# Performance work log

Hardware: AMD Instinct MI355X
Metric: run time of the kernel (lower is better)

## Reference

```python
import jax, jax.numpy as jnp
import numpy as np

N = 100000
E = 3200000
F_IN = 27
H1, C1 = 8, 8
H2, C2 = 1, 2
NEG_SLOPE = 0.2


def gat_conv(x, src, dst, W, a_src, a_dst, b, heads, ch, n_nodes):
    # x: [N, F_in]; src/dst: [E'] (self-loops already appended)
    h = (x @ W).reshape(n_nodes, heads, ch)            # [N, H, C]
    alpha_src = jnp.sum(h * a_src, axis=-1)            # [N, H]
    alpha_dst = jnp.sum(h * a_dst, axis=-1)            # [N, H]
    e = jax.nn.leaky_relu(alpha_src[src] + alpha_dst[dst], NEG_SLOPE)  # [E', H]
    m = jax.ops.segment_max(e, dst, num_segments=n_nodes)             # [N, H]
    ex = jnp.exp(e - m[dst])
    denom = jax.ops.segment_sum(ex, dst, num_segments=n_nodes)        # [N, H]
    alpha = ex / denom[dst]                                           # [E', H]
    out = jax.ops.segment_sum(h[src] * alpha[:, :, None], dst, num_segments=n_nodes)
    return out.reshape(n_nodes, heads * ch) + b


def setup_inputs() -> dict:
    key = jax.random.key(0)
    ks = jax.random.split(key, 10)
    x = jax.random.normal(ks[0], (N, F_IN), dtype=jnp.float32)
    edge_index = jax.random.randint(ks[1], (2, E), 0, N, dtype=jnp.int64)
    s1 = 1.0 / np.sqrt(F_IN)
    s2 = 1.0 / np.sqrt(H1 * C1)
    W1 = jax.random.uniform(ks[2], (F_IN, H1 * C1), jnp.float32, -s1, s1)
    a_src1 = jax.random.uniform(ks[3], (H1, C1), jnp.float32, -s1, s1)
    a_dst1 = jax.random.uniform(ks[4], (H1, C1), jnp.float32, -s1, s1)
    b1 = jnp.zeros((H1 * C1,), jnp.float32)
    W2 = jax.random.uniform(ks[5], (H1 * C1, H2 * C2), jnp.float32, -s2, s2)
    a_src2 = jax.random.uniform(ks[6], (H2, C2), jnp.float32, -s2, s2)
    a_dst2 = jax.random.uniform(ks[7], (H2, C2), jnp.float32, -s2, s2)
    b2 = jnp.zeros((H2 * C2,), jnp.float32)
    return {"x": x, "edge_index": edge_index, "W1": W1, "a_src1": a_src1,
            "a_dst1": a_dst1, "b1": b1, "W2": W2, "a_src2": a_src2,
            "a_dst2": a_dst2, "b2": b2}


def reference(x, edge_index, W1, a_src1, a_dst1, b1, W2, a_src2, a_dst2, b2):
    # eval mode: dropouts are identity. PyG GATConv adds self-loops by default.
    loop = jnp.arange(N, dtype=edge_index.dtype)
    src = jnp.concatenate([edge_index[0], loop])
    dst = jnp.concatenate([edge_index[1], loop])
    h = jax.nn.elu(gat_conv(x, src, dst, W1, a_src1, a_dst1, b1, H1, C1, N))
    out = gat_conv(h, src, dst, W2, a_src2, a_dst2, b2, H2, C2, N)
    return jax.nn.log_softmax(out, axis=1)
```

## Files before the change

kernel.cpp:

```cpp
#include <hip/hip_runtime.h>
#include <hip/hip_fp16.h>
#include <math.h>

#define NN 100000
#define EE 3200000
#define ET (EE + NN)

#define H1n 8
#define C1n 8
#define F1n 64
#define FINn 27
#define NEG 0.2f

#define NPB 128
#define NB 782
#define STRIDE 5120
#define TILE 4096
#define ABLK 256
#define WIN (STRIDE + NPB)
#define FBLK 512

typedef float floatx2 __attribute__((ext_vector_type(2)));

static __device__ __forceinline__ float lrelu(float v) {
    return v > 0.f ? v : NEG * v;
}

__global__ __launch_bounds__(ABLK) void k_binA(const int* __restrict__ ei,
                                               int* __restrict__ tail,
                                               int* __restrict__ recs) {
    __shared__ int hist[NB];
    __shared__ int lofs[NB];
    __shared__ int cur[NB];
    __shared__ int gpos[NB];
    __shared__ int sorted[TILE];
    __shared__ unsigned short sbkt[TILE];
    __shared__ int part[ABLK];

    int tid = threadIdx.x;
    long long e0 = (long long)blockIdx.x * TILE;
    int cnt = (int)min((long long)TILE, (long long)EE - e0);

    for (int i = tid; i < NB; i += ABLK) hist[i] = 0;
    __syncthreads();

    int ss[TILE / ABLK], dd[TILE / ABLK];
    #pragma unroll
    for (int k = 0; k < TILE / ABLK; ++k) {
        int idx = k * ABLK + tid;
        if (idx < cnt) {
            ss[k] = ei[e0 + idx];
            dd[k] = ei[EE + e0 + idx];
            atomicAdd(&hist[dd[k] >> 7], 1);
        }
    }
    __syncthreads();
    {
        const int CH = (NB + ABLK - 1) / ABLK;
        int beg = tid * CH, end = min(beg + CH, NB);
        int s = 0;
        for (int i = beg; i < end; ++i) s += hist[i];
        part[tid] = s;
        __syncthreads();
        for (int off = 1; off < ABLK; off <<= 1) {
            int add = (tid >= off) ? part[tid - off] : 0;
            __syncthreads();
            part[tid] += add;
            __syncthreads();
        }
        int ex = (tid > 0) ? part[tid - 1] : 0;
        for (int i = beg; i < end; ++i) {
            lofs[i] = ex;
            cur[i] = ex;
            ex += hist[i];
        }
    }
    __syncthreads();
    #pragma unroll
    for (int k = 0; k < TILE / ABLK; ++k) {
        int idx = k * ABLK + tid;
        if (idx < cnt) {
            int b = dd[k] >> 7;
            int r = atomicAdd(&cur[b], 1);
            sorted[r] = ss[k] | ((dd[k] & (NPB - 1)) << 17);
            sbkt[r] = (unsigned short)b;
        }
    }
    __syncthreads();
    for (int i = tid; i < NB; i += ABLK) {
        int c = hist[i];
        if (c > 0) gpos[i] = atomicAdd(&tail[i], c);
    }
    __syncthreads();
    for (int t = tid; t < cnt; t += ABLK) {
        int b = sbkt[t];
        recs[(size_t)b * STRIDE + gpos[b] + (t - lofs[b])] = sorted[t];
    }
}

__global__ __launch_bounds__(256) void k_h1(const float* __restrict__ x,
                                            const float* __restrict__ W1,
                                            const float* __restrict__ a_src1,
                                            const float* __restrict__ a_dst1,
                                            unsigned char* __restrict__ h1q,
                                            __half* __restrict__ as1h,
                                            float* __restrict__ ad1) {
    int gt = blockIdx.x * blockDim.x + threadIdx.x;
    int n = gt >> 6;
    if (n >= NN) return;
    int lane = threadIdx.x & 63;
    const float* xr = x + (size_t)n * FINn;
    float s = 0.f;
    #pragma unroll
    for (int k = 0; k < FINn; ++k) s = fmaf(xr[k], W1[k * F1n + lane], s);
    float s2 = __shfl_down(s, 1, 64);
    if (!(lane & 1)) {
        int pk = __builtin_amdgcn_cvt_pk_fp8_f32(s, s2, 0, false);
        ((unsigned short*)(h1q + (size_t)n * F1n))[lane >> 1] =
            (unsigned short)(pk & 0xFFFF);
    }
    float ps = s * a_src1[lane];
    float pd = s * a_dst1[lane];
    #pragma unroll
    for (int off = 1; off < 8; off <<= 1) {
        ps += __shfl_xor(ps, off, 64);
        pd += __shfl_xor(pd, off, 64);
    }
    if ((lane & 7) == 0) {
        int h = lane >> 3;
        as1h[n * H1n + h] = __float2half(ps);
        ad1[n * H1n + h] = pd;
    }
}

__global__ __launch_bounds__(FBLK) void k_f1(const int* __restrict__ recs,
                                             const int* __restrict__ tail,
                                             const unsigned* __restrict__ h1q,
                                             const __half* __restrict__ as1h,
                                             const float* __restrict__ ad1,
                                             const float* __restrict__ b1,
                                             const float* __restrict__ W2,
                                             const float* __restrict__ a_src2,
                                             const float* __restrict__ a_dst2,
                                             uint2* __restrict__ rec2) {
    __shared__ int hist[NPB];
    __shared__ int cur[NPB];
    __shared__ int rloc[NPB + 1];
    __shared__ int window[WIN];
    __shared__ int wtot[2];

    int b = blockIdx.x;
    int tid = threadIdx.x;
    int node0 = b * NPB;
    int nodes = min(NPB, NN - node0);
    int rcnt = tail[b];
    const int* rb = recs + (size_t)b * STRIDE;

    if (tid < NPB) hist[tid] = 0;
    __syncthreads();
    for (int i = tid; i < rcnt; i += FBLK) atomicAdd(&hist[rb[i] >> 17], 1);
    __syncthreads();
    int v = 0, inc = 0;
    if (tid < NPB) {
        v = (tid < nodes) ? hist[tid] + 1 : 0;
        inc = v;
        #pragma unroll
        for (int off = 1; off < 64; off <<= 1) {
            int t = __shfl_up(inc, off, 64);
            if ((tid & 63) >= off) inc += t;
        }
        if ((tid & 63) == 63) wtot[tid >> 6] = inc;
    }
    __syncthreads();
    if (tid < NPB) {
        if (tid >= 64) inc += wtot[0];
        int ex = inc - v;
        if (tid < nodes) {
            rloc[tid] = ex;
            cur[tid] = ex + 1;
            window[ex] = node0 + tid;
        }
    }
    if (tid == 0) rloc[nodes] = wtot[0] + wtot[1];
    __syncthreads();
    for (int i = tid; i < rcnt; i += FBLK) {
        int r = rb[i];
        int p = atomicAdd(&cur[r >> 17], 1);
        window[p] = r & 0x1FFFF;
    }
    __syncthreads();

    int lane = tid & 63;
    int wv = tid >> 6;
    int e8 = lane >> 3;
    int hh = lane & 7;
    int q = lane >> 4;
    int c4 = lane & 15;
    int bpe = e8 << 2;
    int bpq = q << 2;
    int bpx = ((q << 3) + (c4 >> 1)) << 2;

    for (int ln = wv; ln < nodes; ln += FBLK / 64) {
        int n = node0 + ln;
        float adh = ad1[(n << 3) + hh];
        int beg = rloc[ln], end = rloc[ln + 1];
        float a0 = 0.f, a1 = 0.f, a2 = 0.f, a3 = 0.f, den = 0.f;

        for (int base = beg; base < end; base += 64) {
            int cnt = min(64, end - base);
            int sidx = (lane < cnt) ? window[base + lane] : 0;
            for (int sb = 0; sb < cnt; sb += 8) {
                int sb4 = sb << 2;
                int s_sc = __builtin_amdgcn_ds_bpermute(sb4 + bpe, sidx);
                float A = __half2float(as1h[((unsigned)s_sc << 3) + hh]);
                float sc = A + adh;
                sc = fmaxf(sc, 0.2f * sc);
                float x = (sb + e8 < cnt) ? __expf(sc) : 0.f;
                den += x;
                int xi = __float_as_int(x);
                #pragma unroll
                for (int jj = 0; jj < 2; ++jj) {
                    int s_a = __builtin_amdgcn_ds_bpermute(sb4 + (jj << 4) + bpq, sidx);
                    int xr_ = __builtin_amdgcn_ds_bpermute((jj << 7) + bpx, xi);
                    float xv = __int_as_float(xr_);
                    unsigned dw = h1q[((unsigned)s_a << 4) + c4];
                    floatx2 lo = __builtin_amdgcn_cvt_pk_f32_fp8((int)dw, false);
                    floatx2 hi = __builtin_amdgcn_cvt_pk_f32_fp8((int)dw, true);
                    a0 = fmaf(xv, lo.x, a0);
                    a1 = fmaf(xv, lo.y, a1);
                    a2 = fmaf(xv, hi.x, a2);
                    a3 = fmaf(xv, hi.y, a3);
                }
            }
        }

        den += __shfl_xor(den, 8, 64);
        den += __shfl_xor(den, 16, 64);
        den += __shfl_xor(den, 32, 64);
        den = __int_as_float(
            __builtin_amdgcn_ds_bpermute((c4 >> 1) << 2, __float_as_int(den)));
        #pragma unroll
        for (int off = 16; off < 64; off <<= 1) {
            a0 += __shfl_xor(a0, off, 64);
            a1 += __shfl_xor(a1, off, 64);
            a2 += __shfl_xor(a2, off, 64);
            a3 += __shfl_xor(a3, off, 64);
        }
        float inv = 1.f / den;
        float v0 = a0 * inv + b1[c4 * 4 + 0];
        float v1 = a1 * inv + b1[c4 * 4 + 1];
        float v2 = a2 * inv + b1[c4 * 4 + 2];
        float v3 = a3 * inv + b1[c4 * 4 + 3];
        v0 = v0 > 0.f ? v0 : expm1f(v0);
        v1 = v1 > 0.f ? v1 : expm1f(v1);
        v2 = v2 > 0.f ? v2 : expm1f(v2);
        v3 = v3 > 0.f ? v3 : expm1f(v3);
        float p0 = v0 * W2[(c4 * 4 + 0) * 2 + 0] + v1 * W2[(c4 * 4 + 1) * 2 + 0] +
                   v2 * W2[(c4 * 4 + 2) * 2 + 0] + v3 * W2[(c4 * 4 + 3) * 2 + 0];
        float p1 = v0 * W2[(c4 * 4 + 0) * 2 + 1] + v1 * W2[(c4 * 4 + 1) * 2 + 1] +
                   v2 * W2[(c4 * 4 + 2) * 2 + 1] + v3 * W2[(c4 * 4 + 3) * 2 + 1];
        #pragma unroll
        for (int off = 1; off < 16; off <<= 1) {
            p0 += __shfl_xor(p0, off, 64);
            p1 += __shfl_xor(p1, off, 64);
        }
        if (lane == 0) {
            float as2 = p0 * a_src2[0] + p1 * a_src2[1];
            float ad2 = p0 * a_dst2[0] + p1 * a_dst2[1];
            __half2 lo2 = __floats2half2_rn(p0, p1);
            __half2 hi2 = __floats2half2_rn(as2, ad2);
            uint2 r;
            r.x = *(unsigned*)&lo2;
            r.y = *(unsigned*)&hi2;
            rec2[n] = r;
        }
    }
}

__global__ __launch_bounds__(FBLK) void k_f2(const int* __restrict__ recs,
                                             const int* __restrict__ tail,
                                             const uint2* __restrict__ rec2,
                                             const float* __restrict__ b2,
                                             float* __restrict__ out) {
    __shared__ int hist[NPB];
    __shared__ int cur[NPB];
    __shared__ int rloc[NPB + 1];
    __shared__ int window[WIN];
    __shared__ int wtot[2];

    int b = blockIdx.x;
    int tid = threadIdx.x;
    int node0 = b * NPB;
    int nodes = min(NPB, NN - node0);
    int rcnt = tail[b];
    const int* rb = recs + (size_t)b * STRIDE;

    if (tid < NPB) hist[tid] = 0;
    __syncthreads();
    for (int i = tid; i < rcnt; i += FBLK) atomicAdd(&hist[rb[i] >> 17], 1);
    __syncthreads();
    int v = 0, inc = 0;
    if (tid < NPB) {
        v = (tid < nodes) ? hist[tid] + 1 : 0;
        inc = v;
        #pragma unroll
        for (int off = 1; off < 64; off <<= 1) {
            int t = __shfl_up(inc, off, 64);
            if ((tid & 63) >= off) inc += t;
        }
        if ((tid & 63) == 63) wtot[tid >> 6] = inc;
    }
    __syncthreads();
    if (tid < NPB) {
        if (tid >= 64) inc += wtot[0];
        int ex = inc - v;
        if (tid < nodes) {
            rloc[tid] = ex;
            cur[tid] = ex + 1;
            window[ex] = node0 + tid;
        }
    }
    if (tid == 0) rloc[nodes] = wtot[0] + wtot[1];
    __syncthreads();
    for (int i = tid; i < rcnt; i += FBLK) {
        int r = rb[i];
        int p = atomicAdd(&cur[r >> 17], 1);
        window[p] = r & 0x1FFFF;
    }
    __syncthreads();

    int lane = tid & 63;
    int wv = tid >> 6;
    for (int ln = wv; ln < nodes; ln += FBLK / 64) {
        int n = node0 + ln;
        __half2 mysd = *(const __half2*)&rec2[n].y;
        float adv = __half2float(__high2half(mysd));
        int beg = rloc[ln], end = rloc[ln + 1];
        float den = 0.f, a0 = 0.f, a1 = 0.f;
        for (int i = beg + lane; i < end; i += 64) {
            int s = window[i];
            uint2 rv = rec2[s];
            __half2 h01 = *(const __half2*)&rv.x;
            __half2 hsd = *(const __half2*)&rv.y;
            float e = lrelu(__half2float(__low2half(hsd)) + adv);
            float ex = __expf(e);
            den += ex;
            a0 = fmaf(ex, __half2float(__low2half(h01)), a0);
            a1 = fmaf(ex, __half2float(__high2half(h01)), a1);
        }
        #pragma unroll
        for (int off = 32; off > 0; off >>= 1) {
            den += __shfl_xor(den, off, 64);
            a0 += __shfl_xor(a0, off, 64);
            a1 += __shfl_xor(a1, off, 64);
        }
        if (lane == 0) {
            float v0 = a0 / den + b2[0];
            float v1 = a1 / den + b2[1];
            float mx = fmaxf(v0, v1);
            float ls = mx + logf(__expf(v0 - mx) + __expf(v1 - mx));
            out[n * 2 + 0] = v0 - ls;
            out[n * 2 + 1] = v1 - ls;
        }
    }
}

extern "C" void kernel_launch(void* const* d_in, const int* in_sizes, int n_in,
                              void* d_out, int out_size, void* d_ws, size_t ws_size,
                              hipStream_t stream) {
    const float* x      = (const float*)d_in[0];
    const int*   ei     = (const int*)d_in[1];
    const float* W1     = (const float*)d_in[2];
    const float* a_src1 = (const float*)d_in[3];
    const float* a_dst1 = (const float*)d_in[4];
    const float* b1     = (const float*)d_in[5];
    const float* W2     = (const float*)d_in[6];
    const float* a_src2 = (const float*)d_in[7];
    const float* a_dst2 = (const float*)d_in[8];
    const float* b2     = (const float*)d_in[9];
    float* out = (float*)d_out;

    char* wsb = (char*)d_ws;
    size_t o = 0;
    uint2* rec2 = (uint2*)wsb;                   o += (size_t)NN * 8;
    #define ALLOC(name, type, count) type* name = (type*)(wsb + o); o += (size_t)(count) * 4;
    ALLOC(ad1,    float, NN * H1n)
    ALLOC(recs,   int,   (size_t)NB * STRIDE)
    ALLOC(tail,   int,   NB)
    #undef ALLOC
    __half* as1h = (__half*)(wsb + o);               o += (size_t)NN * H1n * 2;
    unsigned char* h1q = (unsigned char*)(wsb + o);  o += (size_t)NN * F1n;

    const int B = 256;
    #define GRID(n) ((unsigned)(((long long)(n) + B - 1) / B))

    hipMemsetAsync(tail, 0, (size_t)NB * sizeof(int), stream);
    k_binA<<<(EE + TILE - 1) / TILE, ABLK, 0, stream>>>(ei, tail, recs);

    k_h1<<<GRID((size_t)NN * 64), B, 0, stream>>>(x, W1, a_src1, a_dst1, h1q, as1h, ad1);

    k_f1<<<NB, FBLK, 0, stream>>>(recs, tail, (const unsigned*)h1q, as1h, ad1, b1,
                                  W2, a_src2, a_dst2, rec2);

    k_f2<<<NB, FBLK, 0, stream>>>(recs, tail, rec2, b2, out);
    #undef GRID
}
```

Baseline: 218.2 us.

## Interleave two nodes per wave in layer-1 gather; use LDS atomics in layer 2

Layer-1 aggregation now processes two destination nodes per wavefront at once to raise memory-level parallelism, with an occupancy hint in launch bounds. Layer-2 aggregation drops the per-block counting sort and window build, and instead accumulates softmax numerator and denominator directly with shared-memory float atomics per destination. Nontemporal loads are used for the streaming edge records. This adds register pressure in layer 1 and relies on the max-free softmax staying in range. LDS atomic contention in layer 2 also makes the summation order nondeterministic.

```diff
diff --git a/kernel.cpp b/kernel.cpp
--- a/kernel.cpp
+++ b/kernel.cpp
@@ -49,8 +49,8 @@
     for (int k = 0; k < TILE / ABLK; ++k) {
         int idx = k * ABLK + tid;
         if (idx < cnt) {
-            ss[k] = ei[e0 + idx];
-            dd[k] = ei[EE + e0 + idx];
+            ss[k] = __builtin_nontemporal_load(&ei[e0 + idx]);
+            dd[k] = __builtin_nontemporal_load(&ei[EE + e0 + idx]);
             atomicAdd(&hist[dd[k] >> 7], 1);
         }
     }
@@ -133,16 +133,16 @@
     }
 }
 
-__global__ __launch_bounds__(FBLK) void k_f1(const int* __restrict__ recs,
-                                             const int* __restrict__ tail,
-                                             const unsigned* __restrict__ h1q,
-                                             const __half* __restrict__ as1h,
-                                             const float* __restrict__ ad1,
-                                             const float* __restrict__ b1,
-                                             const float* __restrict__ W2,
-                                             const float* __restrict__ a_src2,
-                                             const float* __restrict__ a_dst2,
-                                             uint2* __restrict__ rec2) {
+__global__ __launch_bounds__(FBLK, 6) void k_f1(const int* __restrict__ recs,
+                                                const int* __restrict__ tail,
+                                                const unsigned* __restrict__ h1q,
+                                                const __half* __restrict__ as1h,
+                                                const float* __restrict__ ad1,
+                                                const float* __restrict__ b1,
+                                                const float* __restrict__ W2,
+                                                const float* __restrict__ a_src2,
+                                                const float* __restrict__ a_dst2,
+                                                uint2* __restrict__ rec2) {
     __shared__ int hist[NPB];
     __shared__ int cur[NPB];
     __shared__ int rloc[NPB + 1];
@@ -158,7 +158,8 @@
 
     if (tid < NPB) hist[tid] = 0;
     __syncthreads();
-    for (int i = tid; i < rcnt; i += FBLK) atomicAdd(&hist[rb[i] >> 17], 1);
+    for (int i = tid; i < rcnt; i += FBLK)
+        atomicAdd(&hist[__builtin_nontemporal_load(&rb[i]) >> 17], 1);
     __syncthreads();
     int v = 0, inc = 0;
     if (tid < NPB) {
@@ -184,7 +185,7 @@
     if (tid == 0) rloc[nodes] = wtot[0] + wtot[1];
     __syncthreads();
     for (int i = tid; i < rcnt; i += FBLK) {
-        int r = rb[i];
+        int r = __builtin_nontemporal_load(&rb[i]);
         int p = atomicAdd(&cur[r >> 17], 1);
         window[p] = r & 0x1FFFF;
     }
@@ -200,80 +201,117 @@
     int bpq = q << 2;
     int bpx = ((q << 3) + (c4 >> 1)) << 2;
 
-    for (int ln = wv; ln < nodes; ln += FBLK / 64) {
-        int n = node0 + ln;
-        float adh = ad1[(n << 3) + hh];
-        int beg = rloc[ln], end = rloc[ln + 1];
-        float a0 = 0.f, a1 = 0.f, a2 = 0.f, a3 = 0.f, den = 0.f;
-
-        for (int base = beg; base < end; base += 64) {
-            int cnt = min(64, end - base);
-            int sidx = (lane < cnt) ? window[base + lane] : 0;
-            for (int sb = 0; sb < cnt; sb += 8) {
+    for (int m = 0; m < NPB / 16; ++m) {
+        int lnA = wv + (m << 4);
+        int lnB = lnA + 8;
+        bool okA = lnA < nodes, okB = lnB < nodes;
+        if (!okA) break;
+        int nA = node0 + lnA;
+        int nB = node0 + (okB ? lnB : lnA);
+        float adhA = ad1[(nA << 3) + hh];
+        float adhB = ad1[(nB << 3) + hh];
+        int begA = rloc[lnA], endA = rloc[lnA + 1];
+        int begB = okB ? rloc[lnB] : 0, endB = okB ? rloc[lnB + 1] : 0;
+        float a0A = 0.f, a1A = 0.f, a2A = 0.f, a3A = 0.f, denA = 0.f;
+        float a0B = 0.f, a1B = 0.f, a2B = 0.f, a3B = 0.f, denB = 0.f;
+
+        int baseA = begA, baseB = begB;
+        while (baseA < endA || baseB < endB) {
+            int cntA = (baseA < endA) ? min(64, endA - baseA) : 0;
+            int cntB = (baseB < endB) ? min(64, endB - baseB) : 0;
+            int sidxA = (lane < cntA) ? window[baseA + lane] : 0;
+            int sidxB = (lane < cntB) ? window[baseB + lane] : 0;
+            int mx = max(cntA, cntB);
+            for (int sb = 0; sb < mx; sb += 8) {
                 int sb4 = sb << 2;
-                int s_sc = __builtin_amdgcn_ds_bpermute(sb4 + bpe, sidx);
-                float A = __half2float(as1h[((unsigned)s_sc << 3) + hh]);
-                float sc = A + adh;
-                sc = fmaxf(sc, 0.2f * sc);
-                float x = (sb + e8 < cnt) ? __expf(sc) : 0.f;
-                den += x;
-                int xi = __float_as_int(x);
+                int sscA = __builtin_amdgcn_ds_bpermute(sb4 + bpe, sidxA);
+                int sscB = __builtin_amdgcn_ds_bpermute(sb4 + bpe, sidxB);
+                float AA = __half2float(as1h[((unsigned)sscA << 3) + hh]);
+                float AB = __half2float(as1h[((unsigned)sscB << 3) + hh]);
+                float scA = AA + adhA;
+                float scB = AB + adhB;
+                scA = fmaxf(scA, 0.2f * scA);
+                scB = fmaxf(scB, 0.2f * scB);
+                float xA = (sb + e8 < cntA) ? __expf(scA) : 0.f;
+                float xB = (sb + e8 < cntB) ? __expf(scB) : 0.f;
+                denA += xA;
+                denB += xB;
+                int xiA = __float_as_int(xA);
+                int xiB = __float_as_int(xB);
                 #pragma unroll
                 for (int jj = 0; jj < 2; ++jj) {
-                    int s_a = __builtin_amdgcn_ds_bpermute(sb4 + (jj << 4) + bpq, sidx);
-                    int xr_ = __builtin_amdgcn_ds_bpermute((jj << 7) + bpx, xi);
-                    float xv = __int_as_float(xr_);
-                    unsigned dw = h1q[((unsigned)s_a << 4) + c4];
-                    floatx2 lo = __builtin_amdgcn_cvt_pk_f32_fp8((int)dw, false);
-                    floatx2 hi = __builtin_amdgcn_cvt_pk_f32_fp8((int)dw, true);
-                    a0 = fmaf(xv, lo.x, a0);
-                    a1 = fmaf(xv, lo.y, a1);
-                    a2 = fmaf(xv, hi.x, a2);
-                    a3 = fmaf(xv, hi.y, a3);
+                    int saA = __builtin_amdgcn_ds_bpermute(sb4 + (jj << 4) + bpq, sidxA);
+                    int saB = __builtin_amdgcn_ds_bpermute(sb4 + (jj << 4) + bpq, sidxB);
+                    int xrA = __builtin_amdgcn_ds_bpermute((jj << 7) + bpx, xiA);
+                    int xrB = __builtin_amdgcn_ds_bpermute((jj << 7) + bpx, xiB);
+                    unsigned dwA = h1q[((unsigned)saA << 4) + c4];
+                    unsigned dwB = h1q[((unsigned)saB << 4) + c4];
+                    float xvA = __int_as_float(xrA);
+                    float xvB = __int_as_float(xrB);
+                    floatx2 loA = __builtin_amdgcn_cvt_pk_f32_fp8((int)dwA, false);
+                    floatx2 hiA = __builtin_amdgcn_cvt_pk_f32_fp8((int)dwA, true);
+                    floatx2 loB = __builtin_amdgcn_cvt_pk_f32_fp8((int)dwB, false);
+                    floatx2 hiB = __builtin_amdgcn_cvt_pk_f32_fp8((int)dwB, true);
+                    a0A = fmaf(xvA, loA.x, a0A);
+                    a1A = fmaf(xvA, loA.y, a1A);
+                    a2A = fmaf(xvA, hiA.x, a2A);
+                    a3A = fmaf(xvA, hiA.y, a3A);
+                    a0B = fmaf(xvB, loB.x, a0B);
+                    a1B = fmaf(xvB, loB.y, a1B);
+                    a2B = fmaf(xvB, hiB.x, a2B);
+                    a3B = fmaf(xvB, hiB.y, a3B);
                 }
             }
-        }
-
-        den += __shfl_xor(den, 8, 64);
-        den += __shfl_xor(den, 16, 64);
-        den += __shfl_xor(den, 32, 64);
-        den = __int_as_float(
-            __builtin_amdgcn_ds_bpermute((c4 >> 1) << 2, __float_as_int(den)));
-        #pragma unroll
-        for (int off = 16; off < 64; off <<= 1) {
-            a0 += __shfl_xor(a0, off, 64);
-            a1 += __shfl_xor(a1, off, 64);
-            a2 += __shfl_xor(a2, off, 64);
-            a3 += __shfl_xor(a3, off, 64);
-        }
-        float inv = 1.f / den;
-        float v0 = a0 * inv + b1[c4 * 4 + 0];
-        float v1 = a1 * inv + b1[c4 * 4 + 1];
-        float v2 = a2 * inv + b1[c4 * 4 + 2];
-        float v3 = a3 * inv + b1[c4 * 4 + 3];
-        v0 = v0 > 0.f ? v0 : expm1f(v0);
-        v1 = v1 > 0.f ? v1 : expm1f(v1);
-        v2 = v2 > 0.f ? v2 : expm1f(v2);
-        v3 = v3 > 0.f ? v3 : expm1f(v3);
-        float p0 = v0 * W2[(c4 * 4 + 0) * 2 + 0] + v1 * W2[(c4 * 4 + 1) * 2 + 0] +
-                   v2 * W2[(c4 * 4 + 2) * 2 + 0] + v3 * W2[(c4 * 4 + 3) * 2 + 0];
-        float p1 = v0 * W2[(c4 * 4 + 0) * 2 + 1] + v1 * W2[(c4 * 4 + 1) * 2 + 1] +
-                   v2 * W2[(c4 * 4 + 2) * 2 + 1] + v3 * W2[(c4 * 4 + 3) * 2 + 1];
-        #pragma unroll
-        for (int off = 1; off < 16; off <<= 1) {
-            p0 += __shfl_xor(p0, off, 64);
-            p1 += __shfl_xor(p1, off, 64);
-        }
-        if (lane == 0) {
-            float as2 = p0 * a_src2[0] + p1 * a_src2[1];
-            float ad2 = p0 * a_dst2[0] + p1 * a_dst2[1];
-            __half2 lo2 = __floats2half2_rn(p0, p1);
-            __half2 hi2 = __floats2half2_rn(as2, ad2);
-            uint2 r;
-            r.x = *(unsigned*)&lo2;
-            r.y = *(unsigned*)&hi2;
-            rec2[n] = r;
-        }
+            baseA += 64;
+            baseB += 64;
+        }
+
+        #define EPILOGUE(a0, a1, a2, a3, den, n)                                     \
+        {                                                                            \
+            den += __shfl_xor(den, 8, 64);                                           \
+            den += __shfl_xor(den, 16, 64);                                          \
+            den += __shfl_xor(den, 32, 64);                                          \
+            den = __int_as_float(                                                    \
+                __builtin_amdgcn_ds_bpermute((c4 >> 1) << 2, __float_as_int(den)));  \
+            _Pragma("unroll")                                                        \
+            for (int off = 16; off < 64; off <<= 1) {                                \
+                a0 += __shfl_xor(a0, off, 64);                                       \
+                a1 += __shfl_xor(a1, off, 64);                                       \
+                a2 += __shfl_xor(a2, off, 64);                                       \
+                a3 += __shfl_xor(a3, off, 64);                                       \
+            }                                                                        \
+            float inv = 1.f / den;                                                   \
+            float v0 = a0 * inv + b1[c4 * 4 + 0];                                    \
+            float v1 = a1 * inv + b1[c4 * 4 + 1];                                    \
+            float v2 = a2 * inv + b1[c4 * 4 + 2];                                    \
+            float v3 = a3 * inv + b1[c4 * 4 + 3];                                    \
+            v0 = v0 > 0.f ? v0 : expm1f(v0);                                         \
+            v1 = v1 > 0.f ? v1 : expm1f(v1);                                         \
+            v2 = v2 > 0.f ? v2 : expm1f(v2);                                         \
+            v3 = v3 > 0.f ? v3 : expm1f(v3);                                         \
+            float p0 = v0 * W2[(c4 * 4 + 0) * 2 + 0] + v1 * W2[(c4 * 4 + 1) * 2 + 0] \
+                     + v2 * W2[(c4 * 4 + 2) * 2 + 0] + v3 * W2[(c4 * 4 + 3) * 2 + 0];\
+            float p1 = v0 * W2[(c4 * 4 + 0) * 2 + 1] + v1 * W2[(c4 * 4 + 1) * 2 + 1] \
+                     + v2 * W2[(c4 * 4 + 2) * 2 + 1] + v3 * W2[(c4 * 4 + 3) * 2 + 1];\
+            _Pragma("unroll")                                                        \
+            for (int off = 1; off < 16; off <<= 1) {                                 \
+                p0 += __shfl_xor(p0, off, 64);                                       \
+                p1 += __shfl_xor(p1, off, 64);                                       \
+            }                                                                        \
+            if (lane == 0) {                                                         \
+                float as2 = p0 * a_src2[0] + p1 * a_src2[1];                         \
+                float ad2 = p0 * a_dst2[0] + p1 * a_dst2[1];                         \
+                __half2 lo2 = __floats2half2_rn(p0, p1);                             \
+                __half2 hi2 = __floats2half2_rn(as2, ad2);                           \
+                uint2 r;                                                             \
+                r.x = *(unsigned*)&lo2;                                              \
+                r.y = *(unsigned*)&hi2;                                              \
+                rec2[n] = r;                                                         \
+            }                                                                        \
+        }
+        EPILOGUE(a0A, a1A, a2A, a3A, denA, nA)
+        if (okB) EPILOGUE(a0B, a1B, a2B, a3B, denB, nB)
+        #undef EPILOGUE
     }
 }
 
@@ -282,11 +320,8 @@
                                              const uint2* __restrict__ rec2,
                                              const float* __restrict__ b2,
                                              float* __restrict__ out) {
-    __shared__ int hist[NPB];
-    __shared__ int cur[NPB];
-    __shared__ int rloc[NPB + 1];
-    __shared__ int window[WIN];
-    __shared__ int wtot[2];
+    __shared__ float accd[NPB], acc0[NPB], acc1[NPB];
+    __shared__ uint2 myrec[NPB];
 
     int b = blockIdx.x;
     int tid = threadIdx.x;
@@ -295,73 +330,49 @@
     int rcnt = tail[b];
     const int* rb = recs + (size_t)b * STRIDE;
 
-    if (tid < NPB) hist[tid] = 0;
-    __syncthreads();
-    for (int i = tid; i < rcnt; i += FBLK) atomicAdd(&hist[rb[i] >> 17], 1);
-    __syncthreads();
-    int v = 0, inc = 0;
     if (tid < NPB) {
-        v = (tid < nodes) ? hist[tid] + 1 : 0;
-        inc = v;
-        #pragma unroll
-        for (int off = 1; off < 64; off <<= 1) {
-            int t = __shfl_up(inc, off, 64);
-            if ((tid & 63) >= off) inc += t;
-        }
-        if ((tid & 63) == 63) wtot[tid >> 6] = inc;
-    }
-    __syncthreads();
-    if (tid < NPB) {
-        if (tid >= 64) inc += wtot[0];
-        int ex = inc - v;
-        if (tid < nodes) {
-            rloc[tid] = ex;
-            cur[tid] = ex + 1;
-            window[ex] = node0 + tid;
-        }
-    }
-    if (tid == 0) rloc[nodes] = wtot[0] + wtot[1];
-    __syncthreads();
+        accd[tid] = 0.f;
+        acc0[tid] = 0.f;
+        acc1[tid] = 0.f;
+        myrec[tid] = rec2[node0 + min(tid, nodes - 1)];
+    }
+    __syncthreads();
+
     for (int i = tid; i < rcnt; i += FBLK) {
-        int r = rb[i];
-        int p = atomicAdd(&cur[r >> 17], 1);
-        window[p] = r & 0x1FFFF;
-    }
-    __syncthreads();
-
-    int lane = tid & 63;
-    int wv = tid >> 6;
-    for (int ln = wv; ln < nodes; ln += FBLK / 64) {
-        int n = node0 + ln;
-        __half2 mysd = *(const __half2*)&rec2[n].y;
-        float adv = __half2float(__high2half(mysd));
-        int beg = rloc[ln], end = rloc[ln + 1];
-        float den = 0.f, a0 = 0.f, a1 = 0.f;
-        for (int i = beg + lane; i < end; i += 64) {
-            int s = window[i];
-            uint2 rv = rec2[s];
-            __half2 h01 = *(const __half2*)&rv.x;
-            __half2 hsd = *(const __half2*)&rv.y;
-            float e = lrelu(__half2float(__low2half(hsd)) + adv);
-            float ex = __expf(e);
-            den += ex;
-            a0 = fmaf(ex, __half2float(__low2half(h01)), a0);
-            a1 = fmaf(ex, __half2float(__high2half(h01)), a1);
-        }
-        #pragma unroll
-        for (int off = 32; off > 0; off >>= 1) {
-            den += __shfl_xor(den, off, 64);
-            a0 += __shfl_xor(a0, off, 64);
-            a1 += __shfl_xor(a1, off, 64);
-        }
-        if (lane == 0) {
-            float v0 = a0 / den + b2[0];
-            float v1 = a1 / den + b2[1];
-            float mx = fmaxf(v0, v1);
-            float ls = mx + logf(__expf(v0 - mx) + __expf(v1 - mx));
-            out[n * 2 + 0] = v0 - ls;
-            out[n * 2 + 1] = v1 - ls;
-        }
+        int r = __builtin_nontemporal_load(&rb[i]);
+        int s = r & 0x1FFFF;
+        int dL = r >> 17;
+        uint2 rv = rec2[s];
+        __half2 ssd = *(const __half2*)&rv.y;
+        __half2 dsd = *(const __half2*)&myrec[dL].y;
+        float e = lrelu(__half2float(__low2half(ssd)) +
+                        __half2float(__high2half(dsd)));
+        float ex = __expf(e);
+        __half2 h01 = *(const __half2*)&rv.x;
+        atomicAdd(&accd[dL], ex);
+        atomicAdd(&acc0[dL], ex * __half2float(__low2half(h01)));
+        atomicAdd(&acc1[dL], ex * __half2float(__high2half(h01)));
+    }
+    __syncthreads();
+
+    if (tid < nodes) {
+        uint2 rv = myrec[tid];
+        __half2 h01 = *(const __half2*)&rv.x;
+        __half2 hsd = *(const __half2*)&rv.y;
+        float e = lrelu(__half2float(__low2half(hsd)) +
+                        __half2float(__high2half(hsd)));
+        float ex = __expf(e);
+        float den = accd[tid] + ex;
+        float a0 = acc0[tid] + ex * __half2float(__low2half(h01));
+        float a1 = acc1[tid] + ex * __half2float(__high2half(h01));
+        float v0 = a0 / den + b2[0];
+        float v1 = a1 / den + b2[1];
+        float mx = fmaxf(v0, v1);
+        float ls = mx + logf(__expf(v0 - mx) + __expf(v1 - mx));
+        float2 o;
+        o.x = v0 - ls;
+        o.y = v1 - ls;
+        ((float2*)out)[node0 + tid] = o;
     }
 }
 
```

Measured after the change: 262.1 us. 20.2% more time.

## Persist per-block CSR windows from k_f1 and simplify k_f2 to thread-per-node

Applied to the files above, without the earlier changes.

k_f1 now writes its shared-memory grouped source window and per-node ranges to global workspace, and keeps the binned records in registers instead of reloading them for the scatter pass. k_f2 no longer re-histograms and re-scatters the binned edges; each thread walks its node's neighbor list from global memory. This removes the duplicated binning work in the second layer, but trades wave-cooperative coalesced gathers for serial per-thread loops with poorly coalesced index reads and extra global writes.

```diff
diff --git a/kernel.cpp b/kernel.cpp
--- a/kernel.cpp
+++ b/kernel.cpp
@@ -19,6 +19,7 @@
 #define ABLK 256
 #define WIN (STRIDE + NPB)
 #define FBLK 512
+#define RPT 10
 
 typedef float floatx2 __attribute__((ext_vector_type(2)));
 
@@ -142,7 +143,9 @@
                                              const float* __restrict__ W2,
                                              const float* __restrict__ a_src2,
                                              const float* __restrict__ a_dst2,
-                                             uint2* __restrict__ rec2) {
+                                             uint2* __restrict__ rec2,
+                                             int* __restrict__ gwin,
+                                             uint2* __restrict__ nrange) {
     __shared__ int hist[NPB];
     __shared__ int cur[NPB];
     __shared__ int rloc[NPB + 1];
@@ -158,7 +161,17 @@
 
     if (tid < NPB) hist[tid] = 0;
     __syncthreads();
-    for (int i = tid; i < rcnt; i += FBLK) atomicAdd(&hist[rb[i] >> 17], 1);
+    int rg[RPT];
+    int nmine = 0;
+    #pragma unroll
+    for (int k = 0; k < RPT; ++k) {
+        int i = tid + k * FBLK;
+        if (i < rcnt) {
+            rg[k] = rb[i];
+            atomicAdd(&hist[rg[k] >> 17], 1);
+            nmine = k + 1;
+        }
+    }
     __syncthreads();
     int v = 0, inc = 0;
     if (tid < NPB) {
@@ -183,12 +196,27 @@
     }
     if (tid == 0) rloc[nodes] = wtot[0] + wtot[1];
     __syncthreads();
-    for (int i = tid; i < rcnt; i += FBLK) {
-        int r = rb[i];
-        int p = atomicAdd(&cur[r >> 17], 1);
-        window[p] = r & 0x1FFFF;
-    }
-    __syncthreads();
+    #pragma unroll
+    for (int k = 0; k < RPT; ++k) {
+        if (k < nmine) {
+            int r = rg[k];
+            int p = atomicAdd(&cur[r >> 17], 1);
+            window[p] = r & 0x1FFFF;
+        }
+    }
+    __syncthreads();
+    {
+        int T = rloc[nodes];
+        int gbase = b * WIN;
+        for (int i = tid; i < T; i += FBLK)
+            gwin[gbase + i] = window[i];
+        if (tid < nodes) {
+            uint2 r;
+            r.x = (unsigned)(gbase + rloc[tid]);
+            r.y = (unsigned)(gbase + rloc[tid + 1]);
+            nrange[node0 + tid] = r;
+        }
+    }
 
     int lane = tid & 63;
     int wv = tid >> 6;
@@ -277,92 +305,36 @@
     }
 }
 
-__global__ __launch_bounds__(FBLK) void k_f2(const int* __restrict__ recs,
-                                             const int* __restrict__ tail,
-                                             const uint2* __restrict__ rec2,
-                                             const float* __restrict__ b2,
-                                             float* __restrict__ out) {
-    __shared__ int hist[NPB];
-    __shared__ int cur[NPB];
-    __shared__ int rloc[NPB + 1];
-    __shared__ int window[WIN];
-    __shared__ int wtot[2];
-
-    int b = blockIdx.x;
-    int tid = threadIdx.x;
-    int node0 = b * NPB;
-    int nodes = min(NPB, NN - node0);
-    int rcnt = tail[b];
-    const int* rb = recs + (size_t)b * STRIDE;
-
-    if (tid < NPB) hist[tid] = 0;
-    __syncthreads();
-    for (int i = tid; i < rcnt; i += FBLK) atomicAdd(&hist[rb[i] >> 17], 1);
-    __syncthreads();
-    int v = 0, inc = 0;
-    if (tid < NPB) {
-        v = (tid < nodes) ? hist[tid] + 1 : 0;
-        inc = v;
-        #pragma unroll
-        for (int off = 1; off < 64; off <<= 1) {
-            int t = __shfl_up(inc, off, 64);
-            if ((tid & 63) >= off) inc += t;
-        }
-        if ((tid & 63) == 63) wtot[tid >> 6] = inc;
-    }
-    __syncthreads();
-    if (tid < NPB) {
-        if (tid >= 64) inc += wtot[0];
-        int ex = inc - v;
-        if (tid < nodes) {
-            rloc[tid] = ex;
-            cur[tid] = ex + 1;
-            window[ex] = node0 + tid;
-        }
-    }
-    if (tid == 0) rloc[nodes] = wtot[0] + wtot[1];
-    __syncthreads();
-    for (int i = tid; i < rcnt; i += FBLK) {
-        int r = rb[i];
-        int p = atomicAdd(&cur[r >> 17], 1);
-        window[p] = r & 0x1FFFF;
-    }
-    __syncthreads();
-
-    int lane = tid & 63;
-    int wv = tid >> 6;
-    for (int ln = wv; ln < nodes; ln += FBLK / 64) {
-        int n = node0 + ln;
-        __half2 mysd = *(const __half2*)&rec2[n].y;
-        float adv = __half2float(__high2half(mysd));
-        int beg = rloc[ln], end = rloc[ln + 1];
-        float den = 0.f, a0 = 0.f, a1 = 0.f;
-        for (int i = beg + lane; i < end; i += 64) {
-            int s = window[i];
-            uint2 rv = rec2[s];
-            __half2 h01 = *(const __half2*)&rv.x;
-            __half2 hsd = *(const __half2*)&rv.y;
-            float e = lrelu(__half2float(__low2half(hsd)) + adv);
-            float ex = __expf(e);
-            den += ex;
-            a0 = fmaf(ex, __half2float(__low2half(h01)), a0);
-            a1 = fmaf(ex, __half2float(__high2half(h01)), a1);
-        }
-        #pragma unroll
-        for (int off = 32; off > 0; off >>= 1) {
-            den += __shfl_xor(den, off, 64);
-            a0 += __shfl_xor(a0, off, 64);
-            a1 += __shfl_xor(a1, off, 64);
-        }
-        if (lane == 0) {
-            float v0 = a0 / den + b2[0];
-            float v1 = a1 / den + b2[1];
-            float mx = fmaxf(v0, v1);
-            float ls = mx + logf(__expf(v0 - mx) + __expf(v1 - mx));
-            out[n * 2 + 0] = v0 - ls;
-            out[n * 2 + 1] = v1 - ls;
-        }
-    }
+__global__ __launch_bounds__(256) void k_f2(const int* __restrict__ gwin,
+                                            const uint2* __restrict__ nrange,
+                                            const uint2* __restrict__ rec2,
+                                            const float* __restrict__ b2,
+                                            float* __restrict__ out) {
+    int n = blockIdx.x * blockDim.x + threadIdx.x;
+    if (n >= NN) return;
+    __half2 mysd = *(const __half2*)&rec2[n].y;
+    float adv = __half2float(__high2half(mysd));
+    uint2 rr = nrange[n];
+    float den = 0.f, a0 = 0.f, a1 = 0.f;
+    for (unsigned i = rr.x; i < rr.y; ++i) {
+        int s = gwin[i];
+        uint2 rv = rec2[s];
+        __half2 h01 = *(const __half2*)&rv.x;
+        __half2 hsd = *(const __half2*)&rv.y;
+        float e = lrelu(__half2float(__low2half(hsd)) + adv);
+        float ex = __expf(e);
+        den += ex;
+        a0 = fmaf(ex, __half2float(__low2half(h01)), a0);
+        a1 = fmaf(ex, __half2float(__high2half(h01)), a1);
+    }
+    float v0 = a0 / den + b2[0];
+    float v1 = a1 / den + b2[1];
+    float mx = fmaxf(v0, v1);
+    float ls = mx + logf(__expf(v0 - mx) + __expf(v1 - mx));
+    float2 o;
+    o.x = v0 - ls;
+    o.y = v1 - ls;
+    ((float2*)out)[n] = o;
 }
 
 extern "C" void kernel_launch(void* const* d_in, const int* in_sizes, int n_in,
@@ -383,9 +355,11 @@
     char* wsb = (char*)d_ws;
     size_t o = 0;
     uint2* rec2 = (uint2*)wsb;                   o += (size_t)NN * 8;
+    uint2* nrange = (uint2*)(wsb + o);           o += (size_t)NN * 8;
     #define ALLOC(name, type, count) type* name = (type*)(wsb + o); o += (size_t)(count) * 4;
     ALLOC(ad1,    float, NN * H1n)
     ALLOC(recs,   int,   (size_t)NB * STRIDE)
+    ALLOC(gwin,   int,   (size_t)NB * WIN)
     ALLOC(tail,   int,   NB)
     #undef ALLOC
     __half* as1h = (__half*)(wsb + o);               o += (size_t)NN * H1n * 2;
@@ -400,8 +374,8 @@
     k_h1<<<GRID((size_t)NN * 64), B, 0, stream>>>(x, W1, a_src1, a_dst1, h1q, as1h, ad1);
 
     k_f1<<<NB, FBLK, 0, stream>>>(recs, tail, (const unsigned*)h1q, as1h, ad1, b1,
-                                  W2, a_src2, a_dst2, rec2);
-
-    k_f2<<<NB, FBLK, 0, stream>>>(recs, tail, rec2, b2, out);
+                                  W2, a_src2, a_dst2, rec2, gwin, nrange);
+
+    k_f2<<<GRID(NN), B, 0, stream>>>(gwin, nrange, rec2, b2, out);
     #undef GRID
 }
```

New measurement: 217.1 us. About the same (-0.5%).
